# Kernel optimization log

Measured on AMD Instinct MI355X. Metric: run time of the kernel, lower is better.

Reference implementation:

```python
import jax, jax.numpy as jnp
import numpy as np

D = 32       # d_model / hidden_size
H = 4        # n_heads
E = D // H   # head dim = 8
N = 2000     # nodes (hardcoded in FourierBlock weights / proj_class)
L = 96       # seq_len
MODES = (1, 4, 5)  # self.index hardcoded in FourierBlock
KAVG = 25    # moving_avg kernel (first of kernel list; layer uses res[0], trends[0])


def setup_inputs() -> dict:
    key = jax.random.key(0)
    ks = jax.random.split(key, 12)
    B = 8
    x = jax.random.normal(ks[0], (B, N, L, D), jnp.float32)
    lin = lambda k: jax.random.normal(k, (D, D), jnp.float32) * (1.0 / np.sqrt(D))
    scale = 1.0 / (D * D)  # FourierBlock: scale * torch.rand(...)
    W1 = jax.random.uniform(ks[5], (N, H, E, E, len(MODES)), jnp.float32) * scale
    W2 = jax.random.uniform(ks[6], (N, H, E, E, len(MODES)), jnp.float32) * scale
    return {
        "x": x,
        "Wq": lin(ks[1]), "bq": jnp.zeros((D,), jnp.float32),
        "Wk": lin(ks[2]), "bk": jnp.zeros((D,), jnp.float32),
        "Wv": lin(ks[3]), "bv": jnp.zeros((D,), jnp.float32),
        "Wo": lin(ks[4]), "bo": jnp.zeros((D,), jnp.float32),
        "W1": W1, "W2": W2,
    }


def _fourier_block(q, W1, W2):
    # q: [B, N, L, H, E] -> permute to [B, N, H, E, L] (torch: x = q.permute(0,1,3,4,2))
    B, Nn, Ll, Hh, Ee = q.shape
    xq = jnp.transpose(q, (0, 1, 3, 4, 2))
    x_ft = jnp.fft.rfft(xq, axis=-1)                 # [B, N, H, E, L//2+1] complex
    idx = jnp.array(MODES)
    xm = x_ft[..., idx]                              # [B, N, H, E, M]
    Wc = W1 + 1j * W2                                # complex per-node frequency weights
    out_m = jnp.einsum('bnhem,nheom->bnhom', xm, Wc.astype(jnp.complex64))
    F = Ll // 2 + 1
    out_ft = jnp.zeros((B, Nn, Hh, Ee, F), jnp.complex64).at[..., idx].set(out_m)
    y = jnp.fft.irfft(out_ft, n=Ll, axis=-1)         # [B, N, H, E, L]
    return jnp.transpose(y, (0, 1, 4, 2, 3))         # [B, N, L, H, E]


def _moving_avg(x, k):
    # replicate-pad the time axis by (k-1)//2 on each side, then mean over window k (stride 1)
    pad = (k - 1) // 2
    xp = jnp.pad(x, ((0, 0), (0, 0), (pad, pad), (0, 0)), mode='edge')
    cs = jnp.cumsum(xp, axis=2)
    cs = jnp.concatenate([jnp.zeros_like(cs[:, :, :1]), cs], axis=2)
    return (cs[:, :, k:] - cs[:, :, :-k]) / k        # [B, N, T, C]


def reference(x, Wq, bq, Wk, bk, Wv, bv, Wo, bo, W1, W2):
    B, Nn, Ll, Dm = x.shape
    # AutoCorrelationLayer projections
    q = (x @ Wq.T + bq).reshape(B, Nn, Ll, H, E)
    k = (x @ Wk.T + bk).reshape(B, Nn, Ll, H, E)   # faithful: computed, unused by FourierBlock
    v = (x @ Wv.T + bv).reshape(B, Nn, Ll, H, E)   # faithful: computed, unused by FourierBlock
    out = _fourier_block(q, W1, W2)                 # inner_correlation(q, k, v)
    out = out.reshape(B, Nn, Ll, Dm)
    new_x = out @ Wo.T + bo                         # out_projection
    # FFTDecompLayer: residual + series decomposition (eval mode, dropout=0)
    xr = x + new_x
    trend = _moving_avg(xr, KAVG)
    res = xr - trend
    return res
```

## Files before the change

### kernel.cpp

```cpp
#include <hip/hip_runtime.h>


#define N_NODES 2000

__global__ __launch_bounds__(256, 4)
void fused_fourier_decomp(const float* __restrict__ x,
                          const float* __restrict__ Wq,
                          const float* __restrict__ Wo,
                          const float* __restrict__ bo,
                          const float* __restrict__ W1,
                          const float* __restrict__ W2,
                          float* __restrict__ out)
{
  __shared__ __align__(16) float xT[32 * 97];
  __shared__ __align__(16) float basis[96 * 8];
  __shared__ __align__(16) float W12_s[32 * 68];
  __shared__ __align__(16) float Z_s[32 * 8];
  __shared__ float bo_s[32];
  float* const pp  = xT;
  float* const csb = xT + 1600;
  float* const xsb = xT + 1792;
  float* const osb = xT + 1600;

  const int t = threadIdx.x;
  const int bid = blockIdx.x;
  const int n = bid % N_NODES;
  const size_t base = (size_t)bid * (96 * 32);

  const int d = t & 31;
  const int g = t >> 5;
  const int l0 = g * 12;

  float xv[12];
#pragma unroll
  for (int i = 0; i < 12; ++i)
    xv[i] = x[base + (size_t)(l0 + i) * 32 + d];

  {
    const float* W1p = W1 + (size_t)n * 768;
    const float* W2p = W2 + (size_t)n * 768;
    for (int i = t; i < 768; i += 256) {
      const int m = i % 3;
      const int o = (i / 3) & 7;
      const int e = (i / 24) & 7;
      const int h = i / 192;
      const int dst = (h * 8 + o) * 68 + e * 8 + m;
      W12_s[dst]     = W1p[i];
      W12_s[dst + 3] = W2p[i];
    }
  }
  if (t < 32) bo_s[t] = bo[t];

  if (t < 96) {
    const int modes[3] = {1, 4, 5};
#pragma unroll
    for (int m = 0; m < 3; ++m) {
      int r = (modes[m] * t) % 96;
      float ang = (float)r * (6.28318530717958647692f / 96.0f);
      float sv, cv;
      sincosf(ang, &sv, &cv);
      basis[t * 8 + m] = cv;
      basis[t * 8 + 3 + m] = sv;
    }
    basis[t * 8 + 6] = 0.0f;
    basis[t * 8 + 7] = 0.0f;
  }
  __syncthreads();

  {
    float a0 = 0.f, a1 = 0.f, a2 = 0.f, a3 = 0.f, a4 = 0.f, a5 = 0.f;
#pragma unroll
    for (int i = 0; i < 12; ++i) {
      const int l = l0 + i;
      const float4 b0 = *(const float4*)&basis[l * 8];
      const float2 b1 = *(const float2*)&basis[l * 8 + 4];
      const float v = xv[i];
      a0 = fmaf(v, b0.x, a0);
      a1 = fmaf(v, b0.y, a1);
      a2 = fmaf(v, b0.z, a2);
      a3 = fmaf(v, b0.w, a3);
      a4 = fmaf(v, b1.x, a4);
      a5 = fmaf(v, b1.y, a5);
    }
    pp[g * 192 + 0 * 32 + d] = a0;
    pp[g * 192 + 1 * 32 + d] = a1;
    pp[g * 192 + 2 * 32 + d] = a2;
    pp[g * 192 + 3 * 32 + d] = a3;
    pp[g * 192 + 4 * 32 + d] = a4;
    pp[g * 192 + 5 * 32 + d] = a5;
  }
  __syncthreads();

  if (t < 64) {
    const int c  = t & 31;
    const int jj = t >> 5;

    if (t < 48) {
      const int j = t >> 3, cq = t & 7;
      float4 acc = make_float4(0.f, 0.f, 0.f, 0.f);
#pragma unroll
      for (int gg = 0; gg < 8; ++gg) {
        const float4 p = *(const float4*)&pp[gg * 192 + j * 32 + cq * 4];
        acc.x += p.x; acc.y += p.y; acc.z += p.z; acc.w += p.w;
      }
      *(float4*)&csb[j * 32 + cq * 4] = acc;
    }
    __builtin_amdgcn_wave_barrier();

    {
      const float* wqr = Wq + c * 32;
      float4 wq4[8];
#pragma unroll
      for (int q = 0; q < 8; ++q) wq4[q] = *(const float4*)&wqr[q * 4];
      const int jb = jj * 3;
      float X0 = 0.f, X1 = 0.f, X2 = 0.f;
#pragma unroll
      for (int q = 0; q < 8; ++q) {
        const float4 w  = wq4[q];
        const float4 c0 = *(const float4*)&csb[(jb + 0) * 32 + q * 4];
        const float4 c1 = *(const float4*)&csb[(jb + 1) * 32 + q * 4];
        const float4 c2 = *(const float4*)&csb[(jb + 2) * 32 + q * 4];
        X0 = fmaf(w.x, c0.x, X0); X0 = fmaf(w.y, c0.y, X0);
        X0 = fmaf(w.z, c0.z, X0); X0 = fmaf(w.w, c0.w, X0);
        X1 = fmaf(w.x, c1.x, X1); X1 = fmaf(w.y, c1.y, X1);
        X1 = fmaf(w.z, c1.z, X1); X1 = fmaf(w.w, c1.w, X1);
        X2 = fmaf(w.x, c2.x, X2); X2 = fmaf(w.y, c2.y, X2);
        X2 = fmaf(w.z, c2.z, X2); X2 = fmaf(w.w, c2.w, X2);
      }
      const float sgn = jj ? -1.f : 1.f;
      xsb[(jb + 0) * 32 + c] = sgn * X0;
      xsb[(jb + 1) * 32 + c] = sgn * X1;
      xsb[(jb + 2) * 32 + c] = sgn * X2;
    }
    __builtin_amdgcn_wave_barrier();

    {
      const int h = (t >> 3) & 3;
      const int o = t & 7;
      const int cp = h * 8 + o;
      const float* wrow = &W12_s[cp * 68];
      float od0 = 0.f, od1 = 0.f, od2 = 0.f;

#define DSTEP(XC, E_) do {                                                  \
        const float4 wa = *(const float4*)&wrow[(E_) * 8];      \
        const float2 wb = *(const float2*)&wrow[(E_) * 8 + 4];     \
        { const float a = jj ? wa.x : -wa.w; const float b = jj ? wa.w : wa.x;    \
          od0 = fmaf(xr0.XC, b, fmaf(xi0.XC, a, od0)); }                          \
        { const float a = jj ? wa.y : -wb.x; const float b = jj ? wb.x : wa.y;    \
          od1 = fmaf(xr1.XC, b, fmaf(xi1.XC, a, od1)); }                          \
        { const float a = jj ? wa.z : -wb.y; const float b = jj ? wb.y : wa.z;    \
          od2 = fmaf(xr2.XC, b, fmaf(xi2.XC, a, od2)); }                          \
      } while (0)

      {
        const float4 xr0 = *(const float4*)&xsb[0 * 32 + h * 8];
        const float4 xr1 = *(const float4*)&xsb[1 * 32 + h * 8];
        const float4 xr2 = *(const float4*)&xsb[2 * 32 + h * 8];
        const float4 xi0 = *(const float4*)&xsb[3 * 32 + h * 8];
        const float4 xi1 = *(const float4*)&xsb[4 * 32 + h * 8];
        const float4 xi2 = *(const float4*)&xsb[5 * 32 + h * 8];
        DSTEP(x, 0); DSTEP(y, 1); DSTEP(z, 2); DSTEP(w, 3);
      }
      {
        const float4 xr0 = *(const float4*)&xsb[0 * 32 + h * 8 + 4];
        const float4 xr1 = *(const float4*)&xsb[1 * 32 + h * 8 + 4];
        const float4 xr2 = *(const float4*)&xsb[2 * 32 + h * 8 + 4];
        const float4 xi0 = *(const float4*)&xsb[3 * 32 + h * 8 + 4];
        const float4 xi1 = *(const float4*)&xsb[4 * 32 + h * 8 + 4];
        const float4 xi2 = *(const float4*)&xsb[5 * 32 + h * 8 + 4];
        DSTEP(x, 4); DSTEP(y, 5); DSTEP(z, 6); DSTEP(w, 7);
      }
#undef DSTEP

      osb[(jj * 3 + 0) * 32 + cp] = od0;
      osb[(jj * 3 + 1) * 32 + cp] = od1;
      osb[(jj * 3 + 2) * 32 + cp] = od2;
    }
    __builtin_amdgcn_wave_barrier();

    {
      const float* wor = Wo + c * 32;
      float4 wo4[8];
#pragma unroll
      for (int q = 0; q < 8; ++q) wo4[q] = *(const float4*)&wor[q * 4];
      const int jb = jj * 3;
      float Z0 = 0.f, Z1 = 0.f, Z2 = 0.f;
#pragma unroll
      for (int q = 0; q < 8; ++q) {
        const float4 w  = wo4[q];
        const float4 o0 = *(const float4*)&osb[(jb + 0) * 32 + q * 4];
        const float4 o1 = *(const float4*)&osb[(jb + 1) * 32 + q * 4];
        const float4 o2 = *(const float4*)&osb[(jb + 2) * 32 + q * 4];
        Z0 = fmaf(w.x, o0.x, Z0); Z0 = fmaf(w.y, o0.y, Z0);
        Z0 = fmaf(w.z, o0.z, Z0); Z0 = fmaf(w.w, o0.w, Z0);
        Z1 = fmaf(w.x, o1.x, Z1); Z1 = fmaf(w.y, o1.y, Z1);
        Z1 = fmaf(w.z, o1.z, Z1); Z1 = fmaf(w.w, o1.w, Z1);
        Z2 = fmaf(w.x, o2.x, Z2); Z2 = fmaf(w.y, o2.y, Z2);
        Z2 = fmaf(w.z, o2.z, Z2); Z2 = fmaf(w.w, o2.w, Z2);
      }
      Z_s[c * 8 + jb + 0] = Z0;
      Z_s[c * 8 + jb + 1] = Z1;
      Z_s[c * 8 + jb + 2] = Z2;
    }
  }
  __syncthreads();

  float xr[12];
  {
    const float4 z0 = *(const float4*)&Z_s[d * 8];
    const float2 z1 = *(const float2*)&Z_s[d * 8 + 4];
    const float bov = bo_s[d];
#pragma unroll
    for (int i = 0; i < 12; ++i) {
      const int l = l0 + i;
      const float4 b0 = *(const float4*)&basis[l * 8];
      const float2 b1 = *(const float2*)&basis[l * 8 + 4];
      const float v = z0.x * b0.x + z0.y * b0.y + z0.z * b0.z
                    - z0.w * b0.w - z1.x * b1.x - z1.y * b1.y;
      const float r = fmaf(v, (1.0f / 48.0f), bov) + xv[i];
      xr[i] = r;
      xT[d * 97 + l] = r;
    }
  }
  __syncthreads();

  {
    const float* col = &xT[d * 97];
    float lowv[12];
    float S = 0.f;
#pragma unroll
    for (int j = 0; j < 12; ++j) {
      int idx = l0 - 12 + j;
      idx = idx < 0 ? 0 : idx;
      lowv[j] = col[idx];
      S += lowv[j];
    }
#pragma unroll
    for (int i = 0; i < 12; ++i) S += xr[i];
    {
      int idx = l0 + 12;
      idx = idx > 95 ? 95 : idx;
      S += col[idx];
    }
#pragma unroll
    for (int i = 0; i < 12; ++i) {
      const int l = l0 + i;
      const float res = xr[i] - S * (1.0f / 25.0f);
      out[base + (size_t)l * 32 + d] = res;
      int hi = l + 13;
      hi = hi > 95 ? 95 : hi;
      S += col[hi] - lowv[i];
    }
  }
}

extern "C" void kernel_launch(void* const* d_in, const int* in_sizes, int n_in,
                              void* d_out, int out_size, void* d_ws, size_t ws_size,
                              hipStream_t stream) {
  (void)n_in; (void)out_size; (void)d_ws; (void)ws_size;
  const float* x  = (const float*)d_in[0];
  const float* Wq = (const float*)d_in[1];
  const float* Wo = (const float*)d_in[7];
  const float* bo = (const float*)d_in[8];
  const float* W1 = (const float*)d_in[9];
  const float* W2 = (const float*)d_in[10];
  float* out = (float*)d_out;

  const int blocks = in_sizes[0] / (96 * 32);
  fused_fourier_decomp<<<blocks, 256, 0, stream>>>(x, Wq, Wo, bo, W1, W2, out);
}
```

Before: 387.5 us.

## Make blocks persistent per node, loop over batch with prefetch of next tile

Launches one block per node instead of one per (batch,node) tile. Each block stages the node's W1/W2 weights and the basis table in shared memory once, then loops over the 8 batch tiles. While the current tile is being processed, it prefetches the next tile's x values into registers. This removes redundant per-tile weight staging and basis setup and hides global load latency. The cost is a grid of only 2000 blocks, fewer resident waves to hide latency, and extra registers for the prefetch buffer.

```diff
diff --git a/kernel.cpp b/kernel.cpp
--- a/kernel.cpp
+++ b/kernel.cpp
@@ -10,7 +10,8 @@
                           const float* __restrict__ bo,
                           const float* __restrict__ W1,
                           const float* __restrict__ W2,
-                          float* __restrict__ out)
+                          float* __restrict__ out,
+                          const int tiles)
 {
   __shared__ __align__(16) float xT[32 * 97];
   __shared__ __align__(16) float basis[96 * 8];
@@ -23,18 +24,10 @@
   float* const osb = xT + 1600;
 
   const int t = threadIdx.x;
-  const int bid = blockIdx.x;
-  const int n = bid % N_NODES;
-  const size_t base = (size_t)bid * (96 * 32);
-
+  const int n = blockIdx.x;
   const int d = t & 31;
   const int g = t >> 5;
   const int l0 = g * 12;
-
-  float xv[12];
-#pragma unroll
-  for (int i = 0; i < 12; ++i)
-    xv[i] = x[base + (size_t)(l0 + i) * 32 + d];
 
   {
     const float* W1p = W1 + (size_t)n * 768;
@@ -65,81 +58,102 @@
     basis[t * 8 + 6] = 0.0f;
     basis[t * 8 + 7] = 0.0f;
   }
+
+  float xv[12];
+  if (n < tiles) {
+    const float* xp = x + (size_t)n * (96 * 32);
+#pragma unroll
+    for (int i = 0; i < 12; ++i)
+      xv[i] = xp[(size_t)(l0 + i) * 32 + d];
+  }
   __syncthreads();
 
-  {
-    float a0 = 0.f, a1 = 0.f, a2 = 0.f, a3 = 0.f, a4 = 0.f, a5 = 0.f;
-#pragma unroll
-    for (int i = 0; i < 12; ++i) {
-      const int l = l0 + i;
-      const float4 b0 = *(const float4*)&basis[l * 8];
-      const float2 b1 = *(const float2*)&basis[l * 8 + 4];
-      const float v = xv[i];
-      a0 = fmaf(v, b0.x, a0);
-      a1 = fmaf(v, b0.y, a1);
-      a2 = fmaf(v, b0.z, a2);
-      a3 = fmaf(v, b0.w, a3);
-      a4 = fmaf(v, b1.x, a4);
-      a5 = fmaf(v, b1.y, a5);
-    }
-    pp[g * 192 + 0 * 32 + d] = a0;
-    pp[g * 192 + 1 * 32 + d] = a1;
-    pp[g * 192 + 2 * 32 + d] = a2;
-    pp[g * 192 + 3 * 32 + d] = a3;
-    pp[g * 192 + 4 * 32 + d] = a4;
-    pp[g * 192 + 5 * 32 + d] = a5;
-  }
-  __syncthreads();
-
-  if (t < 64) {
-    const int c  = t & 31;
-    const int jj = t >> 5;
-
-    if (t < 48) {
-      const int j = t >> 3, cq = t & 7;
-      float4 acc = make_float4(0.f, 0.f, 0.f, 0.f);
-#pragma unroll
-      for (int gg = 0; gg < 8; ++gg) {
-        const float4 p = *(const float4*)&pp[gg * 192 + j * 32 + cq * 4];
-        acc.x += p.x; acc.y += p.y; acc.z += p.z; acc.w += p.w;
-      }
-      *(float4*)&csb[j * 32 + cq * 4] = acc;
-    }
-    __builtin_amdgcn_wave_barrier();
+  for (int b = 0; b * N_NODES + n < tiles; ++b) {
+    const size_t tile = (size_t)b * N_NODES + n;
+    const size_t base = tile * (96 * 32);
 
     {
-      const float* wqr = Wq + c * 32;
-      float4 wq4[8];
-#pragma unroll
-      for (int q = 0; q < 8; ++q) wq4[q] = *(const float4*)&wqr[q * 4];
-      const int jb = jj * 3;
-      float X0 = 0.f, X1 = 0.f, X2 = 0.f;
-#pragma unroll
-      for (int q = 0; q < 8; ++q) {
-        const float4 w  = wq4[q];
-        const float4 c0 = *(const float4*)&csb[(jb + 0) * 32 + q * 4];
-        const float4 c1 = *(const float4*)&csb[(jb + 1) * 32 + q * 4];
-        const float4 c2 = *(const float4*)&csb[(jb + 2) * 32 + q * 4];
-        X0 = fmaf(w.x, c0.x, X0); X0 = fmaf(w.y, c0.y, X0);
-        X0 = fmaf(w.z, c0.z, X0); X0 = fmaf(w.w, c0.w, X0);
-        X1 = fmaf(w.x, c1.x, X1); X1 = fmaf(w.y, c1.y, X1);
-        X1 = fmaf(w.z, c1.z, X1); X1 = fmaf(w.w, c1.w, X1);
-        X2 = fmaf(w.x, c2.x, X2); X2 = fmaf(w.y, c2.y, X2);
-        X2 = fmaf(w.z, c2.z, X2); X2 = fmaf(w.w, c2.w, X2);
-      }
-      const float sgn = jj ? -1.f : 1.f;
-      xsb[(jb + 0) * 32 + c] = sgn * X0;
-      xsb[(jb + 1) * 32 + c] = sgn * X1;
-      xsb[(jb + 2) * 32 + c] = sgn * X2;
-    }
-    __builtin_amdgcn_wave_barrier();
-
-    {
-      const int h = (t >> 3) & 3;
-      const int o = t & 7;
-      const int cp = h * 8 + o;
-      const float* wrow = &W12_s[cp * 68];
-      float od0 = 0.f, od1 = 0.f, od2 = 0.f;
+      float a0 = 0.f, a1 = 0.f, a2 = 0.f, a3 = 0.f, a4 = 0.f, a5 = 0.f;
+#pragma unroll
+      for (int i = 0; i < 12; ++i) {
+        const int l = l0 + i;
+        const float4 b0 = *(const float4*)&basis[l * 8];
+        const float2 b1 = *(const float2*)&basis[l * 8 + 4];
+        const float v = xv[i];
+        a0 = fmaf(v, b0.x, a0);
+        a1 = fmaf(v, b0.y, a1);
+        a2 = fmaf(v, b0.z, a2);
+        a3 = fmaf(v, b0.w, a3);
+        a4 = fmaf(v, b1.x, a4);
+        a5 = fmaf(v, b1.y, a5);
+      }
+      pp[g * 192 + 0 * 32 + d] = a0;
+      pp[g * 192 + 1 * 32 + d] = a1;
+      pp[g * 192 + 2 * 32 + d] = a2;
+      pp[g * 192 + 3 * 32 + d] = a3;
+      pp[g * 192 + 4 * 32 + d] = a4;
+      pp[g * 192 + 5 * 32 + d] = a5;
+    }
+    __syncthreads();
+
+    float xv2[12];
+    const bool havenext = (tile + N_NODES) < (size_t)tiles;
+    if (havenext) {
+      const float* xp = x + base + (size_t)N_NODES * (96 * 32);
+#pragma unroll
+      for (int i = 0; i < 12; ++i)
+        xv2[i] = xp[(size_t)(l0 + i) * 32 + d];
+    }
+
+    if (t < 64) {
+      const int c  = t & 31;
+      const int jj = t >> 5;
+
+      if (t < 48) {
+        const int j = t >> 3, cq = t & 7;
+        float4 acc = make_float4(0.f, 0.f, 0.f, 0.f);
+#pragma unroll
+        for (int gg = 0; gg < 8; ++gg) {
+          const float4 p = *(const float4*)&pp[gg * 192 + j * 32 + cq * 4];
+          acc.x += p.x; acc.y += p.y; acc.z += p.z; acc.w += p.w;
+        }
+        *(float4*)&csb[j * 32 + cq * 4] = acc;
+      }
+      __builtin_amdgcn_wave_barrier();
+
+      {
+        const float* wqr = Wq + c * 32;
+        float4 wq4[8];
+#pragma unroll
+        for (int q = 0; q < 8; ++q) wq4[q] = *(const float4*)&wqr[q * 4];
+        const int jb = jj * 3;
+        float X0 = 0.f, X1 = 0.f, X2 = 0.f;
+#pragma unroll
+        for (int q = 0; q < 8; ++q) {
+          const float4 w  = wq4[q];
+          const float4 c0 = *(const float4*)&csb[(jb + 0) * 32 + q * 4];
+          const float4 c1 = *(const float4*)&csb[(jb + 1) * 32 + q * 4];
+          const float4 c2 = *(const float4*)&csb[(jb + 2) * 32 + q * 4];
+          X0 = fmaf(w.x, c0.x, X0); X0 = fmaf(w.y, c0.y, X0);
+          X0 = fmaf(w.z, c0.z, X0); X0 = fmaf(w.w, c0.w, X0);
+          X1 = fmaf(w.x, c1.x, X1); X1 = fmaf(w.y, c1.y, X1);
+          X1 = fmaf(w.z, c1.z, X1); X1 = fmaf(w.w, c1.w, X1);
+          X2 = fmaf(w.x, c2.x, X2); X2 = fmaf(w.y, c2.y, X2);
+          X2 = fmaf(w.z, c2.z, X2); X2 = fmaf(w.w, c2.w, X2);
+        }
+        const float sgn = jj ? -1.f : 1.f;
+        xsb[(jb + 0) * 32 + c] = sgn * X0;
+        xsb[(jb + 1) * 32 + c] = sgn * X1;
+        xsb[(jb + 2) * 32 + c] = sgn * X2;
+      }
+      __builtin_amdgcn_wave_barrier();
+
+      {
+        const int h = (t >> 3) & 3;
+        const int o = t & 7;
+        const int cp = h * 8 + o;
+        const float* wrow = &W12_s[cp * 68];
+        float od0 = 0.f, od1 = 0.f, od2 = 0.f;
 
 #define DSTEP(XC, E_) do {                                                  \
         const float4 wa = *(const float4*)&wrow[(E_) * 8];      \
@@ -152,105 +166,110 @@
           od2 = fmaf(xr2.XC, b, fmaf(xi2.XC, a, od2)); }                          \
       } while (0)
 
-      {
-        const float4 xr0 = *(const float4*)&xsb[0 * 32 + h * 8];
-        const float4 xr1 = *(const float4*)&xsb[1 * 32 + h * 8];
-        const float4 xr2 = *(const float4*)&xsb[2 * 32 + h * 8];
-        const float4 xi0 = *(const float4*)&xsb[3 * 32 + h * 8];
-        const float4 xi1 = *(const float4*)&xsb[4 * 32 + h * 8];
-        const float4 xi2 = *(const float4*)&xsb[5 * 32 + h * 8];
-        DSTEP(x, 0); DSTEP(y, 1); DSTEP(z, 2); DSTEP(w, 3);
-      }
-      {
-        const float4 xr0 = *(const float4*)&xsb[0 * 32 + h * 8 + 4];
-        const float4 xr1 = *(const float4*)&xsb[1 * 32 + h * 8 + 4];
-        const float4 xr2 = *(const float4*)&xsb[2 * 32 + h * 8 + 4];
-        const float4 xi0 = *(const float4*)&xsb[3 * 32 + h * 8 + 4];
-        const float4 xi1 = *(const float4*)&xsb[4 * 32 + h * 8 + 4];
-        const float4 xi2 = *(const float4*)&xsb[5 * 32 + h * 8 + 4];
-        DSTEP(x, 4); DSTEP(y, 5); DSTEP(z, 6); DSTEP(w, 7);
-      }
+        {
+          const float4 xr0 = *(const float4*)&xsb[0 * 32 + h * 8];
+          const float4 xr1 = *(const float4*)&xsb[1 * 32 + h * 8];
+          const float4 xr2 = *(const float4*)&xsb[2 * 32 + h * 8];
+          const float4 xi0 = *(const float4*)&xsb[3 * 32 + h * 8];
+          const float4 xi1 = *(const float4*)&xsb[4 * 32 + h * 8];
+          const float4 xi2 = *(const float4*)&xsb[5 * 32 + h * 8];
+          DSTEP(x, 0); DSTEP(y, 1); DSTEP(z, 2); DSTEP(w, 3);
+        }
+        {
+          const float4 xr0 = *(const float4*)&xsb[0 * 32 + h * 8 + 4];
+          const float4 xr1 = *(const float4*)&xsb[1 * 32 + h * 8 + 4];
+          const float4 xr2 = *(const float4*)&xsb[2 * 32 + h * 8 + 4];
+          const float4 xi0 = *(const float4*)&xsb[3 * 32 + h * 8 + 4];
+          const float4 xi1 = *(const float4*)&xsb[4 * 32 + h * 8 + 4];
+          const float4 xi2 = *(const float4*)&xsb[5 * 32 + h * 8 + 4];
+          DSTEP(x, 4); DSTEP(y, 5); DSTEP(z, 6); DSTEP(w, 7);
+        }
 #undef DSTEP
 
-      osb[(jj * 3 + 0) * 32 + cp] = od0;
-      osb[(jj * 3 + 1) * 32 + cp] = od1;
-      osb[(jj * 3 + 2) * 32 + cp] = od2;
-    }
-    __builtin_amdgcn_wave_barrier();
-
+        osb[(jj * 3 + 0) * 32 + cp] = od0;
+        osb[(jj * 3 + 1) * 32 + cp] = od1;
+        osb[(jj * 3 + 2) * 32 + cp] = od2;
+      }
+      __builtin_amdgcn_wave_barrier();
+
+      {
+        const float* wor = Wo + c * 32;
+        float4 wo4[8];
+#pragma unroll
+        for (int q = 0; q < 8; ++q) wo4[q] = *(const float4*)&wor[q * 4];
+        const int jb = jj * 3;
+        float Z0 = 0.f, Z1 = 0.f, Z2 = 0.f;
+#pragma unroll
+        for (int q = 0; q < 8; ++q) {
+          const float4 w  = wo4[q];
+          const float4 o0 = *(const float4*)&osb[(jb + 0) * 32 + q * 4];
+          const float4 o1 = *(const float4*)&osb[(jb + 1) * 32 + q * 4];
+          const float4 o2 = *(const float4*)&osb[(jb + 2) * 32 + q * 4];
+          Z0 = fmaf(w.x, o0.x, Z0); Z0 = fmaf(w.y, o0.y, Z0);
+          Z0 = fmaf(w.z, o0.z, Z0); Z0 = fmaf(w.w, o0.w, Z0);
+          Z1 = fmaf(w.x, o1.x, Z1); Z1 = fmaf(w.y, o1.y, Z1);
+          Z1 = fmaf(w.z, o1.z, Z1); Z1 = fmaf(w.w, o1.w, Z1);
+          Z2 = fmaf(w.x, o2.x, Z2); Z2 = fmaf(w.y, o2.y, Z2);
+          Z2 = fmaf(w.z, o2.z, Z2); Z2 = fmaf(w.w, o2.w, Z2);
+        }
+        Z_s[c * 8 + jb + 0] = Z0;
+        Z_s[c * 8 + jb + 1] = Z1;
+        Z_s[c * 8 + jb + 2] = Z2;
+      }
+    }
+    __syncthreads();
+
+    float xr[12];
     {
-      const float* wor = Wo + c * 32;
-      float4 wo4[8];
-#pragma unroll
-      for (int q = 0; q < 8; ++q) wo4[q] = *(const float4*)&wor[q * 4];
-      const int jb = jj * 3;
-      float Z0 = 0.f, Z1 = 0.f, Z2 = 0.f;
-#pragma unroll
-      for (int q = 0; q < 8; ++q) {
-        const float4 w  = wo4[q];
-        const float4 o0 = *(const float4*)&osb[(jb + 0) * 32 + q * 4];
-        const float4 o1 = *(const float4*)&osb[(jb + 1) * 32 + q * 4];
-        const float4 o2 = *(const float4*)&osb[(jb + 2) * 32 + q * 4];
-        Z0 = fmaf(w.x, o0.x, Z0); Z0 = fmaf(w.y, o0.y, Z0);
-        Z0 = fmaf(w.z, o0.z, Z0); Z0 = fmaf(w.w, o0.w, Z0);
-        Z1 = fmaf(w.x, o1.x, Z1); Z1 = fmaf(w.y, o1.y, Z1);
-        Z1 = fmaf(w.z, o1.z, Z1); Z1 = fmaf(w.w, o1.w, Z1);
-        Z2 = fmaf(w.x, o2.x, Z2); Z2 = fmaf(w.y, o2.y, Z2);
-        Z2 = fmaf(w.z, o2.z, Z2); Z2 = fmaf(w.w, o2.w, Z2);
-      }
-      Z_s[c * 8 + jb + 0] = Z0;
-      Z_s[c * 8 + jb + 1] = Z1;
-      Z_s[c * 8 + jb + 2] = Z2;
-    }
-  }
-  __syncthreads();
-
-  float xr[12];
-  {
-    const float4 z0 = *(const float4*)&Z_s[d * 8];
-    const float2 z1 = *(const float2*)&Z_s[d * 8 + 4];
-    const float bov = bo_s[d];
-#pragma unroll
-    for (int i = 0; i < 12; ++i) {
-      const int l = l0 + i;
-      const float4 b0 = *(const float4*)&basis[l * 8];
-      const float2 b1 = *(const float2*)&basis[l * 8 + 4];
-      const float v = z0.x * b0.x + z0.y * b0.y + z0.z * b0.z
-                    - z0.w * b0.w - z1.x * b1.x - z1.y * b1.y;
-      const float r = fmaf(v, (1.0f / 48.0f), bov) + xv[i];
-      xr[i] = r;
-      xT[d * 97 + l] = r;
-    }
-  }
-  __syncthreads();
-
-  {
-    const float* col = &xT[d * 97];
-    float lowv[12];
-    float S = 0.f;
-#pragma unroll
-    for (int j = 0; j < 12; ++j) {
-      int idx = l0 - 12 + j;
-      idx = idx < 0 ? 0 : idx;
-      lowv[j] = col[idx];
-      S += lowv[j];
-    }
-#pragma unroll
-    for (int i = 0; i < 12; ++i) S += xr[i];
+      const float4 z0 = *(const float4*)&Z_s[d * 8];
+      const float2 z1 = *(const float2*)&Z_s[d * 8 + 4];
+      const float bov = bo_s[d];
+#pragma unroll
+      for (int i = 0; i < 12; ++i) {
+        const int l = l0 + i;
+        const float4 b0 = *(const float4*)&basis[l * 8];
+        const float2 b1 = *(const float2*)&basis[l * 8 + 4];
+        const float v = z0.x * b0.x + z0.y * b0.y + z0.z * b0.z
+                      - z0.w * b0.w - z1.x * b1.x - z1.y * b1.y;
+        const float r = fmaf(v, (1.0f / 48.0f), bov) + xv[i];
+        xr[i] = r;
+        xT[d * 97 + l] = r;
+      }
+    }
+    __syncthreads();
+
     {
-      int idx = l0 + 12;
-      idx = idx > 95 ? 95 : idx;
-      S += col[idx];
-    }
-#pragma unroll
-    for (int i = 0; i < 12; ++i) {
-      const int l = l0 + i;
-      const float res = xr[i] - S * (1.0f / 25.0f);
-      out[base + (size_t)l * 32 + d] = res;
-      int hi = l + 13;
-      hi = hi > 95 ? 95 : hi;
-      S += col[hi] - lowv[i];
-    }
+      const float* col = &xT[d * 97];
+      float lowv[12];
+      float S = 0.f;
+#pragma unroll
+      for (int j = 0; j < 12; ++j) {
+        int idx = l0 - 12 + j;
+        idx = idx < 0 ? 0 : idx;
+        lowv[j] = col[idx];
+        S += lowv[j];
+      }
+#pragma unroll
+      for (int i = 0; i < 12; ++i) S += xr[i];
+      {
+        int idx = l0 + 12;
+        idx = idx > 95 ? 95 : idx;
+        S += col[idx];
+      }
+#pragma unroll
+      for (int i = 0; i < 12; ++i) {
+        const int l = l0 + i;
+        const float res = xr[i] - S * (1.0f / 25.0f);
+        out[base + (size_t)l * 32 + d] = res;
+        int hi = l + 13;
+        hi = hi > 95 ? 95 : hi;
+        S += col[hi] - lowv[i];
+      }
+    }
+    __syncthreads();
+
+#pragma unroll
+    for (int i = 0; i < 12; ++i) xv[i] = xv2[i];
   }
 }
 
@@ -266,6 +285,7 @@
   const float* W2 = (const float*)d_in[10];
   float* out = (float*)d_out;
 
-  const int blocks = in_sizes[0] / (96 * 32);
-  fused_fourier_decomp<<<blocks, 256, 0, stream>>>(x, Wq, Wo, bo, W1, W2, out);
+  const int tiles = in_sizes[0] / (96 * 32);
+  fused_fourier_decomp<<<N_NODES, 256, 0, stream>>>(x, Wq, Wo, bo, W1, W2, out,
+                                                    tiles);
 }
```

Measured after the change: 770.0 us. 98.7% more time.
